# Performance work log

Measured on AMD Instinct MI355X. Metric: run time of the kernel, lower is better.

The kernel has to match this reference:

```python
import jax, jax.numpy as jnp
from jax import lax
import numpy as np

N, I, O = 64, 8, 8
B = 512
S_EX, S_PHI, S_RHO = 10, 60, 60  # S_phi must equal S_rho (alpha loops feed S_rho-sized h into the GRUs)
N_ACTIONS, N_ROLES = 5, 7


def _gru(x, h, Wih, Whh, bih, bhh):
    # torch.nn.GRUCell math
    gi = x @ Wih.T + bih
    gh = h @ Whh.T + bhh
    ir, iz, inn = jnp.split(gi, 3, axis=-1)
    hr, hz, hn = jnp.split(gh, 3, axis=-1)
    r = jax.nn.sigmoid(ir + hr)
    zg = jax.nn.sigmoid(iz + hz)
    n = jnp.tanh(inn + r * hn)
    return (1.0 - zg) * n + zg * h


def setup_inputs() -> dict:
    key = jax.random.key(0)
    ks = jax.random.split(key, 24)
    f32 = jnp.float32
    z = jax.random.normal(ks[0], (B, N, S_EX), f32)
    dz = jax.random.normal(ks[1], (B, N, S_EX), f32)
    has = (jax.random.uniform(ks[2], (B, N)) < 0.9).astype(f32)
    adj = (jnp.triu(jax.random.uniform(ks[3], (N, N)), 1) > 0.7).astype(jnp.int32)

    def lin(k, o, i):
        return (jax.random.normal(k, (o, i), f32) * np.float32(1.0 / np.sqrt(i)))

    d = dict(z=z, dz=dz, has=has, adj=adj)
    d['Wih_f'] = lin(ks[4], 3 * S_PHI, S_RHO)
    d['Whh_f'] = lin(ks[5], 3 * S_PHI, S_PHI)
    d['bih_f'] = jax.random.normal(ks[6], (3 * S_PHI,), f32) * 0.02
    d['bhh_f'] = jax.random.normal(ks[7], (3 * S_PHI,), f32) * 0.02
    d['Wih_b'] = lin(ks[8], 3 * S_PHI, S_RHO)
    d['Whh_b'] = lin(ks[9], 3 * S_PHI, S_PHI)
    d['bih_b'] = jax.random.normal(ks[10], (3 * S_PHI,), f32) * 0.02
    d['bhh_b'] = jax.random.normal(ks[11], (3 * S_PHI,), f32) * 0.02
    d['Wf'] = lin(ks[12], S_RHO, S_PHI + 2 * S_EX)
    d['bf'] = jax.random.normal(ks[13], (S_RHO,), f32) * 0.02
    d['Wb'] = lin(ks[14], S_RHO, S_PHI + 2 * S_EX)
    d['bb'] = jax.random.normal(ks[15], (S_RHO,), f32) * 0.02
    d['Wa'] = lin(ks[16], N_ACTIONS, 2 * S_PHI)
    d['ba'] = jax.random.normal(ks[17], (N_ACTIONS,), f32) * 0.02
    d['Wc'] = lin(ks[18], 1, 2 * S_PHI)
    d['bc'] = jax.random.normal(ks[19], (1,), f32) * 0.02
    d['Wu'] = lin(ks[20], N_ROLES, 2 * S_RHO)
    d['bu'] = jax.random.normal(ks[21], (N_ROLES,), f32) * 0.02
    return d


def reference(z, dz, has, adj,
              Wih_f, Whh_f, bih_f, bhh_f,
              Wih_b, Whh_b, bih_b, bhh_b,
              Wf, bf, Wb, bb, Wa, ba, Wc, bc, Wu, bu):
    Bn, Nn = has.shape
    dt = z.dtype
    adjf = adj.astype(dt)

    # ---- forward sweep over nodes in ascending order ----
    def fwd_outer(rho, i):
        def inner(h, j):
            hn = _gru(rho[j], h, Wih_f, Whh_f, bih_f, bhh_f)
            blend = adjf[j, i] * has[:, j][:, None]  # edge exists AND source node present
            return h + blend * (hn - h), None
        h, _ = lax.scan(inner, jnp.zeros((Bn, S_PHI), dt), jnp.arange(Nn))
        rho_i = jnp.tanh(jnp.concatenate([h, z[:, i], dz[:, i]], 1) @ Wf.T + bf)
        return rho.at[i].set(rho_i), None

    rho_f, _ = lax.scan(fwd_outer, jnp.zeros((Nn, Bn, S_RHO), dt), jnp.arange(Nn))

    # ---- backward sweep over nodes in descending order ----
    def bwd_outer(rho, i):
        def inner(h, j):
            hn = _gru(rho[j], h, Wih_b, Whh_b, bih_b, bhh_b)
            blend = adjf[i, j] * has[:, j][:, None]  # out-edges of i, visited descending
            return h + blend * (hn - h), None
        h, _ = lax.scan(inner, jnp.zeros((Bn, S_PHI), dt), jnp.arange(Nn - 1, -1, -1))
        rho_i = jnp.concatenate([h, z[:, i], dz[:, i]], 1) @ Wb.T + bb
        return rho.at[i].set(rho_i), None

    rho_b, _ = lax.scan(bwd_outer, jnp.zeros((Nn, Bn, S_RHO), dt), jnp.arange(Nn - 1, -1, -1))

    # ---- aggregate outputs (last O nodes) and inputs (first I nodes) ----
    h = jnp.zeros((Bn, S_RHO), dt)
    for i in range(N - O, N):
        hn = _gru(rho_f[i], h, Wih_f, Whh_f, bih_f, bhh_f)
        h = h + has[:, i][:, None] * (hn - h)
    alpha_f = h
    h = jnp.zeros((Bn, S_RHO), dt)
    for i in reversed(range(I)):
        hn = _gru(rho_b[i], h, Wih_b, Whh_b, bih_b, bhh_b)
        h = h + has[:, i][:, None] * (hn - h)
    alpha_b = h

    ab = jnp.concatenate([alpha_f, alpha_b], 1)
    omega = ab @ Wa.T + ba          # [B, 5]
    value = ab @ Wc.T + bc          # [B, 1]

    feats = jnp.concatenate([rho_f, rho_b], -1)           # [N, B, 2*S_rho]
    psi = jnp.einsum('nbs,rs->brn', feats, Wu) + bu[None, :, None]  # [B, 7, N]
    m = has[:, None, :]
    psi = -60.0 * (1.0 - m) + psi * m  # interpolate(-60, psi, has)

    instr_prob = jax.nn.softmax(omega, axis=1)
    role_prob = jax.nn.softmax(psi, axis=2)
    return instr_prob, role_prob, value
```

## Files before the change

### kernel.cpp

```cpp
#include <hip/hip_runtime.h>
#include <hip/hip_bf16.h>

#define NN 64
#define BATCH 512
#define SP 60
#define SG 180
#define SEX 10
#define CATD 80
#define NA 5
#define NR 7
#define OO 8
#define II 8

typedef unsigned long long u64;
typedef unsigned short u16;
typedef unsigned int u32;
typedef unsigned char u8;

#define OFF_Z     0
#define OFF_DZ    327680
#define OFF_HAS   655360
#define OFF_WIHF  688128
#define OFF_WHHF  698928
#define OFF_BIHF  709728
#define OFF_BHHF  709908
#define OFF_WIHB  710088
#define OFF_WHHB  720888
#define OFF_BIHB  731688
#define OFF_BHHB  731868
#define OFF_WF    732048
#define OFF_BF    736848
#define OFF_WB    736908
#define OFF_BB    741708
#define OFF_WA    741768
#define OFF_BA    742368
#define OFF_WC    742373
#define OFF_BC    742493
#define OFF_WU    742494
#define OFF_BU    743334
#define CONV_TOTAL 743341
#define OFF_FLAG  743342
#define OFF_RHOF  743344
#define OFF_RHOB  (OFF_RHOF + 1966080)
#define OFF_ALF   (OFF_RHOB + 1966080)
#define OFF_ALB   (OFF_ALF + 30720)
#define OUT_TOTAL 232448

typedef _Float16 f16;
typedef _Float16 half2_t __attribute__((ext_vector_type(2)));
typedef _Float16 f16x8 __attribute__((ext_vector_type(8)));
typedef float f32x4 __attribute__((ext_vector_type(4)));

__device__ __forceinline__ float us2f(u16 v){
  return __uint_as_float(((u32)v) << 16);
}
__device__ __forceinline__ u16 f2bf(float f){
  __hip_bfloat16 h = __float2bfloat16(f);
  return *reinterpret_cast<u16*>(&h);
}
__device__ __forceinline__ float rcp_(float x){ return __builtin_amdgcn_rcpf(x); }
__device__ __forceinline__ float sigm(float x){
  return rcp_(1.f + __expf(-x));
}
__device__ __forceinline__ float tanh_(float x){
  float e = __expf(2.f*fabsf(x));
  float t = 1.f - 2.f*rcp_(e + 1.f);
  return copysignf(t, x);
}
__device__ __forceinline__ u32 pack2(float a, float b){
  half2_t h; h[0] = (f16)a; h[1] = (f16)b;
  return __builtin_bit_cast(u32, h);
}
__device__ __forceinline__ float fdot2_(u32 a, u32 b, float c){
  return __builtin_amdgcn_fdot2(__builtin_bit_cast(half2_t, a),
                                __builtin_bit_cast(half2_t, b), c, false);
}
__device__ __forceinline__ f16x8 bc16(uint4 v){ return __builtin_bit_cast(f16x8, v); }
__device__ __forceinline__ f32x4 mfma16(f16x8 a, f16x8 b, f32x4 c){
  return __builtin_amdgcn_mfma_f32_16x16x32_f16(a, b, c, 0, 0, 0);
}

struct HP { uint4 q[8]; };
__device__ __forceinline__ u32 hpc(const HP& p, int k){
  const uint4& v = p.q[k>>2];
  switch(k&3){ case 0: return v.x; case 1: return v.y; case 2: return v.z; default: return v.w; }
}

__device__ __forceinline__ int detect_bf16(const u32* w){
  int f = 0;
  for (int i=0;i<256;i++) f |= (w[i] == 0x3F803F80u) ? 1 : 0;
  return f;
}

__global__ __launch_bounds__(256) void conv_in(
  const void* z, const void* dz, const void* has,
  const void* WihF, const void* WhhF, const void* bihF, const void* bhhF,
  const void* WihB, const void* WhhB, const void* bihB, const void* bhhB,
  const void* Wf_, const void* bf_, const void* Wb_, const void* bb_,
  const void* Wa, const void* ba, const void* Wc, const void* bc,
  const void* Wu, const void* bu, float* ws)
{
  const int isbf = detect_bf16((const u32*)has);
  if (blockIdx.x == 0 && threadIdx.x == 0) ws[OFF_FLAG] = (float)isbf;
  int idx = blockIdx.x*256 + threadIdx.x;
  if (idx >= CONV_TOTAL) return;
  const void* src; int loc;
  if      (idx < OFF_DZ  ){ src=z;    loc=idx-OFF_Z;    }
  else if (idx < OFF_HAS ){ src=dz;   loc=idx-OFF_DZ;   }
  else if (idx < OFF_WIHF){ src=has;  loc=idx-OFF_HAS;  }
  else if (idx < OFF_WHHF){ src=WihF; loc=idx-OFF_WIHF; }
  else if (idx < OFF_BIHF){ src=WhhF; loc=idx-OFF_WHHF; }
  else if (idx < OFF_BHHF){ src=bihF; loc=idx-OFF_BIHF; }
  else if (idx < OFF_WIHB){ src=bhhF; loc=idx-OFF_BHHF; }
  else if (idx < OFF_WHHB){ src=WihB; loc=idx-OFF_WIHB; }
  else if (idx < OFF_BIHB){ src=WhhB; loc=idx-OFF_WHHB; }
  else if (idx < OFF_BHHB){ src=bihB; loc=idx-OFF_BIHB; }
  else if (idx < OFF_WF  ){ src=bhhB; loc=idx-OFF_BHHB; }
  else if (idx < OFF_BF  ){ src=Wf_;  loc=idx-OFF_WF;   }
  else if (idx < OFF_WB  ){ src=bf_;  loc=idx-OFF_BF;   }
  else if (idx < OFF_BB  ){ src=Wb_;  loc=idx-OFF_WB;   }
  else if (idx < OFF_WA  ){ src=bb_;  loc=idx-OFF_BB;   }
  else if (idx < OFF_BA  ){ src=Wa;   loc=idx-OFF_WA;   }
  else if (idx < OFF_WC  ){ src=ba;   loc=idx-OFF_BA;   }
  else if (idx < OFF_BC  ){ src=Wc;   loc=idx-OFF_WC;   }
  else if (idx < OFF_WU  ){ src=bc;   loc=idx-OFF_BC;   }
  else if (idx < OFF_BU  ){ src=Wu;   loc=idx-OFF_WU;   }
  else                    { src=bu;   loc=idx-OFF_BU;   }
  float v = isbf ? us2f(((const u16*)src)[loc]) : ((const float*)src)[loc];
  ws[idx] = v;
}

__global__ __launch_bounds__(128, 2) void dir_kernel(const int* __restrict__ adj,
                                                     float* __restrict__ ws)
{
  const int tid = threadIdx.x;
  const int w   = tid >> 6;
  const int u   = tid & 63;
  const int ml  = u & 15;
  const int q   = u >> 4;
  const int bid = blockIdx.x;
  const int bwd = bid >> 9;
  const int b   = bid & 511;

  const float* Wih  = ws + (bwd ? OFF_WIHB : OFF_WIHF);
  const float* Whh  = ws + (bwd ? OFF_WHHB : OFF_WHHF);
  const float* bih  = ws + (bwd ? OFF_BIHB : OFF_BIHF);
  const float* bhh  = ws + (bwd ? OFF_BHHB : OFF_BHHF);
  const float* Wcat = ws + (bwd ? OFF_WB   : OFF_WF);
  const float* bcat = ws + (bwd ? OFF_BB   : OFF_BF);
  const float* zc   = ws + OFF_Z;
  const float* dzc  = ws + OFF_DZ;
  const float* hasc = ws + OFF_HAS;
  float* rho   = ws + (bwd ? OFF_RHOB : OFF_RHOF);
  float* alpha = ws + (bwd ? OFF_ALB  : OFF_ALF);

  __shared__ uint4 sH4[65][9];
  __shared__ uint4 sRhoPad[8];
  __shared__ uint4 sRhoHist[8][8];
  __shared__ float sRhoOut[NN][SP];
  __shared__ u32 sZp[NN][5];
  __shared__ u32 sDZp[NN][5];
  __shared__ float sHas[NN];
  __shared__ u64 sRowM[NN];
  __shared__ u8 sConsL[NN][64];
  __shared__ int sConsCnt[NN];

  #define ROWB(I) ((char*)&sH4[(I)][0])
  const u32 BIASW = 0x3C000000u;

  {
    if (tid < 64){
      u64 rowm = 0;
      for (int j=0;j<64;j++) rowm |= ((u64)(adj[tid*64+j]!=0))<<j;
      sRowM[tid] = rowm;
      sHas[tid] = hasc[b*NN + tid];
    }
    for (int idx=tid; idx<65*9; idx+=128){
      uint4 v = {0,0,0,0};
      if (idx % 9 == 7) v.w = BIASW;
      ((uint4*)sH4)[idx] = v;
    }
    if (tid < 8){ uint4 v={0,0,0,0}; if (tid==7) v.w = BIASW; sRhoPad[tid]=v; }
    if (tid < 64){ uint4 v={0,0,0,0}; if ((tid&7)==7) v.w = BIASW; ((uint4*)sRhoHist)[tid]=v; }
    for (int idx=tid; idx<NN*5; idx+=128){
      int n2=idx/5, p2=idx%5;
      sZp [n2][p2] = pack2(zc [(size_t)b*NN*SEX + n2*SEX + 2*p2],
                           zc [(size_t)b*NN*SEX + n2*SEX + 2*p2+1]);
      sDZp[n2][p2] = pack2(dzc[(size_t)b*NN*SEX + n2*SEX + 2*p2],
                           dzc[(size_t)b*NN*SEX + n2*SEX + 2*p2+1]);
    }
  }
  __syncthreads();
  if (tid < 64){
    u64 cm = 0;
    if (bwd) for (int i2=0;i2<64;i2++) cm |= ((sRowM[i2]>>tid)&1ULL)<<i2;
    u64 m = bwd ? cm : sRowM[tid];
    int c = 0;
    while (m){ int i2 = (int)__builtin_ctzll(m); m &= m-1; sConsL[tid][c++] = (u8)i2; }
    sConsCnt[tid] = c;
  }

  f16x8 Ar[2][4], Az[2][4], Anh[2][2], Ani[2][2];
  #pragma unroll
  for (int mtl=0; mtl<2; mtl++){
    const int mt = 2*w + mtl;
    const int R = 16*mt + ml;
    const bool rok = (R < SP);
    #pragma unroll
    for (int kt=0; kt<4; kt++){
      f16x8 vr, vz;
      #pragma unroll
      for (int j=0;j<8;j++){
        const int K = 32*kt + 8*q + j;
        float wr=0.f, wz=0.f;
        if (rok){
          if (K < SP){ wr = Whh[R*SP+K]; wz = Whh[(60+R)*SP+K]; }
          else if (K >= 64 && K < 64+SP){ wr = Wih[R*SP+(K-64)]; wz = Wih[(60+R)*SP+(K-64)]; }
          else if (K == 127){ wr = bhh[R]+bih[R]; wz = bhh[60+R]+bih[60+R]; }
        }
        vr[j]=(f16)wr; vz[j]=(f16)wz;
      }
      Ar[mtl][kt]=vr; Az[mtl][kt]=vz;
    }
    #pragma unroll
    for (int kt=0; kt<2; kt++){
      f16x8 vn, vi;
      #pragma unroll
      for (int j=0;j<8;j++){
        const int K = 32*kt + 8*q + j;
        float wn=0.f, wi=0.f;
        if (rok){
          if (K < SP){ wn = Whh[(120+R)*SP+K]; wi = Wih[(120+R)*SP+K]; }
          else if (K == 63){ wn = bhh[120+R]; wi = bih[120+R]; }
        }
        vn[j]=(f16)wn; vi[j]=(f16)wi;
      }
      Anh[mtl][kt]=vn; Ani[mtl][kt]=vi;
    }
  }

  u32 wc[40];
  float bct = 0.f;
  if (w == 0){
    #pragma unroll
    for (int k=0;k<40;k++) wc[k] = pack2(Wcat[u*CATD + 2*k], Wcat[u*CATD + 2*k+1]);
    bct = bcat[u];
  }
  __syncthreads();

  auto gatepass = [&](f16x8 Bh0, f16x8 Bh1, f16x8 Br0, f16x8 Br1,
                      const f32x4* Gn, int ci, bool wr, float bl){
    f32x4 Dr[2], Dz[2], Dn[2];
    #pragma unroll
    for (int mtl=0;mtl<2;mtl++){
      f32x4 a={0,0,0,0};
      a = mfma16(Ar[mtl][0], Bh0, a); a = mfma16(Ar[mtl][1], Bh1, a);
      a = mfma16(Ar[mtl][2], Br0, a); a = mfma16(Ar[mtl][3], Br1, a);
      Dr[mtl] = a;
      f32x4 c2={0,0,0,0};
      c2 = mfma16(Az[mtl][0], Bh0, c2); c2 = mfma16(Az[mtl][1], Bh1, c2);
      c2 = mfma16(Az[mtl][2], Br0, c2); c2 = mfma16(Az[mtl][3], Br1, c2);
      Dz[mtl] = c2;
      f32x4 d={0,0,0,0};
      d = mfma16(Anh[mtl][0], Bh0, d); d = mfma16(Anh[mtl][1], Bh1, d);
      Dn[mtl] = d;
    }
    #pragma unroll
    for (int mtl=0;mtl<2;mtl++){
      const int mt = 2*w + mtl;
      char* rp = ROWB(ci) + 32*mt + 8*q;
      uint2 h2 = *(uint2*)rp;
      half2_t ha = __builtin_bit_cast(half2_t, h2.x);
      half2_t hb = __builtin_bit_cast(half2_t, h2.y);
      float hold[4] = { (float)ha[0], (float)ha[1], (float)hb[0], (float)hb[1] };
      float hw[4];
      #pragma unroll
      for (int reg=0;reg<4;reg++){
        float r_ = sigm(Dr[mtl][reg]);
        float zg = sigm(Dz[mtl][reg]);
        float nv = tanh_(Gn[mtl][reg] + r_*Dn[mtl][reg]);
        float hn_ = (1.f - zg)*nv + zg*hold[reg];
        hw[reg] = (bl != 0.f) ? hn_ : hold[reg];
      }
      if (wr && !(mt==3 && q==3)){
        uint2 o; o.x = pack2(hw[0],hw[1]); o.y = pack2(hw[2],hw[3]);
        *(uint2*)rp = o;
      }
    }
  };

  int t = bwd ? 63 : 0;
  const int dt = bwd ? -1 : 1;
  for (int s=0; s<64; s++, t+=dt){
    if (w == 0){
      HP ht;
      { const uint4* _r=(const uint4*)&sH4[t][0];
        #pragma unroll
        for (int _k=0;_k<8;_k++) ht.q[_k]=_r[_k]; }
      float c0 = bct, c1 = 0.f, c2 = 0.f, c3 = 0.f;
      #pragma unroll
      for (int k=0;k<28;k+=4){
        c0 = fdot2_(wc[k],   hpc(ht,k),   c0);
        c1 = fdot2_(wc[k+1], hpc(ht,k+1), c1);
        c2 = fdot2_(wc[k+2], hpc(ht,k+2), c2);
        c3 = fdot2_(wc[k+3], hpc(ht,k+3), c3);
      }
      c0 = fdot2_(wc[28], hpc(ht,28), c0);
      c1 = fdot2_(wc[29], hpc(ht,29), c1);
      #pragma unroll
      for (int p2=0;p2<5;p2++){
        c2 = fdot2_(wc[30+p2], sZp [t][p2], c2);
        c3 = fdot2_(wc[35+p2], sDZp[t][p2], c3);
      }
      float acc = (c0 + c1) + (c2 + c3);
      float rv = bwd ? acc : tanh_(acc);
      if (u < SP){
        sRhoOut[t][u] = rv;
        *(f16*)((char*)&sRhoPad[0] + 2*u) = (f16)rv;
      }
      const int slot = bwd ? t : (t - (NN-OO));
      if (slot >= 0 && slot < 8 && u < SP)
        *(f16*)((char*)&sRhoHist[slot][0] + 2*u) = (f16)rv;
    }
    __syncthreads();

    const float blendT = sHas[t];
    const int cnt = sConsCnt[t];
    if (blendT != 0.f && cnt > 0){
      const f16x8 Br0 = bc16(sRhoPad[q]);
      const f16x8 Br1 = bc16(sRhoPad[4+q]);
      f32x4 Gn[2];
      #pragma unroll
      for (int mtl=0;mtl<2;mtl++){
        f32x4 g={0,0,0,0};
        g = mfma16(Ani[mtl][0], Br0, g);
        g = mfma16(Ani[mtl][1], Br1, g);
        Gn[mtl] = g;
      }
      const int np = (cnt + 15) >> 4;
      for (int p=0; p<np; p++){
        const int idxp = 16*p + ml;
        const int ci = (idxp < cnt) ? (int)sConsL[t][idxp] : 64;
        const f16x8 Bh0 = bc16(sH4[ci][q]);
        const f16x8 Bh1 = bc16(sH4[ci][4+q]);
        __syncthreads();
        gatepass(Bh0, Bh1, Br0, Br1, Gn, ci, idxp < cnt, 1.0f);
      }
    }
    __syncthreads();
  }

  for (int idx=tid; idx<NN*SP; idx+=128){
    int n2 = idx/SP, s2 = idx%SP;
    rho[((size_t)n2*BATCH + b)*SP + s2] = sRhoOut[n2][s2];
  }

  for (int s2=0; s2<8; s2++){
    const int i = bwd ? (7 - s2) : (NN - OO + s2);
    const int slot = bwd ? i : (i - (NN-OO));
    const f16x8 Th0 = bc16(sH4[64][q]);
    const f16x8 Th1 = bc16(sH4[64][4+q]);
    const f16x8 Tr0 = bc16(sRhoHist[slot][q]);
    const f16x8 Tr1 = bc16(sRhoHist[slot][4+q]);
    f32x4 Gt[2];
    #pragma unroll
    for (int mtl=0;mtl<2;mtl++){
      f32x4 g={0,0,0,0};
      g = mfma16(Ani[mtl][0], Tr0, g);
      g = mfma16(Ani[mtl][1], Tr1, g);
      Gt[mtl] = g;
    }
    __syncthreads();
    gatepass(Th0, Th1, Tr0, Tr1, Gt, 64, ml==0, sHas[i]);
    __syncthreads();
  }
  if (tid < SP) alpha[(size_t)b*SP + tid] = (float)*(const f16*)(ROWB(64) + 2*tid);
  #undef ROWB
}

__global__ __launch_bounds__(256, 1) void head_kernel(float* __restrict__ ws,
                                                      void* __restrict__ outp)
{
  const int b = blockIdx.x;
  const int tid = threadIdx.x;
  const int isbf = (ws[OFF_FLAG] != 0.f);
  const float* hasc   = ws + OFF_HAS;
  const float* WaC    = ws + OFF_WA;
  const float* baC    = ws + OFF_BA;
  const float* WcC    = ws + OFF_WC;
  const float* bcC    = ws + OFF_BC;
  const float* WuC    = ws + OFF_WU;
  const float* buC    = ws + OFF_BU;
  const float* rhoF   = ws + OFF_RHOF;
  const float* rhoB   = ws + OFF_RHOB;
  const float* alphaF = ws + OFF_ALF;
  const float* alphaB = ws + OFF_ALB;

  __shared__ float sF[NN][121];
  __shared__ float sAB[120];
  __shared__ float sWu[NR*120];
  __shared__ float sHasR[NN];
  __shared__ float sPsi[NR][NN];
  __shared__ float sRed[NR][2];
  __shared__ float sOm[NA];

  auto wout = [&](int idx, float v){
    if (isbf) ((u16*)outp)[idx] = f2bf(v);
    else      ((float*)outp)[idx] = v;
  };

  for (int idx=tid; idx<NN*SP; idx+=256){
    int n = idx/SP, s = idx%SP;
    sF[n][s]    = rhoF[((size_t)n*BATCH + b)*SP + s];
    sF[n][60+s] = rhoB[((size_t)n*BATCH + b)*SP + s];
  }
  for (int idx=tid; idx<120; idx+=256)
    sAB[idx] = (idx<60) ? alphaF[(size_t)b*SP + idx] : alphaB[(size_t)b*SP + idx-60];
  for (int idx=tid; idx<NR*120; idx+=256) sWu[idx] = WuC[idx];
  for (int idx=tid; idx<NN; idx+=256) sHasR[idx] = hasc[b*NN + idx];
  __syncthreads();

  for (int idx=tid; idx<NR*NN; idx+=256){
    int r = idx/NN, n = idx%NN;
    float acc = buC[r];
    for (int s=0;s<120;s++) acc += sF[n][s]*sWu[r*120+s];
    sPsi[r][n] = (sHasR[n] != 0.f) ? acc : -60.f;
  }
  if (tid >= 64 && tid < 64+NA){
    int a = tid - 64;
    float acc = baC[a];
    for (int s=0;s<120;s++) acc += sAB[s]*WaC[a*120+s];
    sOm[a] = acc;
  }
  if (tid == 70){
    float acc = bcC[0];
    for (int s=0;s<120;s++) acc += sAB[s]*WcC[s];
    wout(2560 + BATCH*NR*NN + b, acc);
  }
  __syncthreads();

  if (tid < NR){
    float m = -1e30f;
    for (int n=0;n<NN;n++) m = fmaxf(m, sPsi[tid][n]);
    float ssum = 0.f;
    for (int n=0;n<NN;n++) ssum += __expf(sPsi[tid][n]-m);
    sRed[tid][0] = m; sRed[tid][1] = 1.f/ssum;
  }
  if (tid == 8){
    float m = -1e30f;
    for (int a=0;a<NA;a++) m = fmaxf(m, sOm[a]);
    float e[NA]; float ssum = 0.f;
    for (int a=0;a<NA;a++){ e[a] = __expf(sOm[a]-m); ssum += e[a]; }
    for (int a=0;a<NA;a++) wout(b*NA + a, e[a]/ssum);
  }
  __syncthreads();

  for (int idx=tid; idx<NR*NN; idx+=256){
    int r = idx/NN, n = idx%NN;
    float v = __expf(sPsi[r][n]-sRed[r][0]) * sRed[r][1];
    wout(2560 + (size_t)b*NR*NN + idx, v);
  }
}

extern "C" void kernel_launch(void* const* d_in, const int* in_sizes, int n_in,
                              void* d_out, int out_size, void* d_ws, size_t ws_size,
                              hipStream_t stream)
{
  const int* adj = (const int*)d_in[3];
  float* ws = (float*)d_ws;

  conv_in<<<(CONV_TOTAL+255)/256, 256, 0, stream>>>(
      d_in[0], d_in[1], d_in[2],
      d_in[4], d_in[5], d_in[6], d_in[7],
      d_in[8], d_in[9], d_in[10], d_in[11],
      d_in[12], d_in[13], d_in[14], d_in[15],
      d_in[16], d_in[17], d_in[18], d_in[19],
      d_in[20], d_in[21], ws);

  dir_kernel<<<1024, 128, 0, stream>>>(adj, ws);

  head_kernel<<<512, 256, 0, stream>>>(ws, d_out);
}
```

Measured before the change: 274.3 us.

## Split GRU gate row tiles across four waves instead of two per block

Doubles the dir_kernel block from 128 to 256 threads, so each of four waves owns one 16-row MFMA tile instead of two. This halves the per-wave MFMA and gate-activation work on the serial recurrence critical path and the weight registers each wave holds. In exchange, every __syncthreads now has twice as many waves to coordinate, and the launch bounds of 256 threads with 4 blocks per unit may force register limits.

Result: slower. 281.9 us (+2.8%).

```diff
diff --git a/kernel.cpp b/kernel.cpp
--- a/kernel.cpp
+++ b/kernel.cpp
@@ -130,7 +130,7 @@
   ws[idx] = v;
 }
 
-__global__ __launch_bounds__(128, 2) void dir_kernel(const int* __restrict__ adj,
+__global__ __launch_bounds__(256, 4) void dir_kernel(const int* __restrict__ adj,
                                                      float* __restrict__ ws)
 {
   const int tid = threadIdx.x;
@@ -175,14 +175,14 @@
       sRowM[tid] = rowm;
       sHas[tid] = hasc[b*NN + tid];
     }
-    for (int idx=tid; idx<65*9; idx+=128){
+    for (int idx=tid; idx<65*9; idx+=256){
       uint4 v = {0,0,0,0};
       if (idx % 9 == 7) v.w = BIASW;
       ((uint4*)sH4)[idx] = v;
     }
     if (tid < 8){ uint4 v={0,0,0,0}; if (tid==7) v.w = BIASW; sRhoPad[tid]=v; }
     if (tid < 64){ uint4 v={0,0,0,0}; if ((tid&7)==7) v.w = BIASW; ((uint4*)sRhoHist)[tid]=v; }
-    for (int idx=tid; idx<NN*5; idx+=128){
+    for (int idx=tid; idx<NN*5; idx+=256){
       int n2=idx/5, p2=idx%5;
       sZp [n2][p2] = pack2(zc [(size_t)b*NN*SEX + n2*SEX + 2*p2],
                            zc [(size_t)b*NN*SEX + n2*SEX + 2*p2+1]);
@@ -200,11 +200,9 @@
     sConsCnt[tid] = c;
   }
 
-  f16x8 Ar[2][4], Az[2][4], Anh[2][2], Ani[2][2];
-  #pragma unroll
-  for (int mtl=0; mtl<2; mtl++){
-    const int mt = 2*w + mtl;
-    const int R = 16*mt + ml;
+  f16x8 Ar[4], Az[4], Anh[2], Ani[2];
+  {
+    const int R = 16*w + ml;
     const bool rok = (R < SP);
     #pragma unroll
     for (int kt=0; kt<4; kt++){
@@ -220,7 +218,7 @@
         }
         vr[j]=(f16)wr; vz[j]=(f16)wz;
       }
-      Ar[mtl][kt]=vr; Az[mtl][kt]=vz;
+      Ar[kt]=vr; Az[kt]=vz;
     }
     #pragma unroll
     for (int kt=0; kt<2; kt++){
@@ -235,7 +233,7 @@
         }
         vn[j]=(f16)wn; vi[j]=(f16)wi;
       }
-      Anh[mtl][kt]=vn; Ani[mtl][kt]=vi;
+      Anh[kt]=vn; Ani[kt]=vi;
     }
   }
 
@@ -249,43 +247,31 @@
   __syncthreads();
 
   auto gatepass = [&](f16x8 Bh0, f16x8 Bh1, f16x8 Br0, f16x8 Br1,
-                      const f32x4* Gn, int ci, bool wr, float bl){
-    f32x4 Dr[2], Dz[2], Dn[2];
+                      f32x4 Gn, int ci, bool wr, float bl){
+    f32x4 Dr={0,0,0,0}, Dz={0,0,0,0}, Dn={0,0,0,0};
+    Dr = mfma16(Ar[0], Bh0, Dr); Dr = mfma16(Ar[1], Bh1, Dr);
+    Dr = mfma16(Ar[2], Br0, Dr); Dr = mfma16(Ar[3], Br1, Dr);
+    Dz = mfma16(Az[0], Bh0, Dz); Dz = mfma16(Az[1], Bh1, Dz);
+    Dz = mfma16(Az[2], Br0, Dz); Dz = mfma16(Az[3], Br1, Dz);
+    Dn = mfma16(Anh[0], Bh0, Dn); Dn = mfma16(Anh[1], Bh1, Dn);
+
+    char* rp = ROWB(ci) + 32*w + 8*q;
+    uint2 h2 = *(uint2*)rp;
+    half2_t ha = __builtin_bit_cast(half2_t, h2.x);
+    half2_t hb = __builtin_bit_cast(half2_t, h2.y);
+    float hold[4] = { (float)ha[0], (float)ha[1], (float)hb[0], (float)hb[1] };
+    float hw[4];
     #pragma unroll
-    for (int mtl=0;mtl<2;mtl++){
-      f32x4 a={0,0,0,0};
-      a = mfma16(Ar[mtl][0], Bh0, a); a = mfma16(Ar[mtl][1], Bh1, a);
-      a = mfma16(Ar[mtl][2], Br0, a); a = mfma16(Ar[mtl][3], Br1, a);
-      Dr[mtl] = a;
-      f32x4 c2={0,0,0,0};
-      c2 = mfma16(Az[mtl][0], Bh0, c2); c2 = mfma16(Az[mtl][1], Bh1, c2);
-      c2 = mfma16(Az[mtl][2], Br0, c2); c2 = mfma16(Az[mtl][3], Br1, c2);
-      Dz[mtl] = c2;
-      f32x4 d={0,0,0,0};
-      d = mfma16(Anh[mtl][0], Bh0, d); d = mfma16(Anh[mtl][1], Bh1, d);
-      Dn[mtl] = d;
-    }
-    #pragma unroll
-    for (int mtl=0;mtl<2;mtl++){
-      const int mt = 2*w + mtl;
-      char* rp = ROWB(ci) + 32*mt + 8*q;
-      uint2 h2 = *(uint2*)rp;
-      half2_t ha = __builtin_bit_cast(half2_t, h2.x);
-      half2_t hb = __builtin_bit_cast(half2_t, h2.y);
-      float hold[4] = { (float)ha[0], (float)ha[1], (float)hb[0], (float)hb[1] };
-      float hw[4];
-      #pragma unroll
-      for (int reg=0;reg<4;reg++){
-        float r_ = sigm(Dr[mtl][reg]);
-        float zg = sigm(Dz[mtl][reg]);
-        float nv = tanh_(Gn[mtl][reg] + r_*Dn[mtl][reg]);
-        float hn_ = (1.f - zg)*nv + zg*hold[reg];
-        hw[reg] = (bl != 0.f) ? hn_ : hold[reg];
-      }
-      if (wr && !(mt==3 && q==3)){
-        uint2 o; o.x = pack2(hw[0],hw[1]); o.y = pack2(hw[2],hw[3]);
-        *(uint2*)rp = o;
-      }
+    for (int reg=0;reg<4;reg++){
+      float r_ = sigm(Dr[reg]);
+      float zg = sigm(Dz[reg]);
+      float nv = tanh_(Gn[reg] + r_*Dn[reg]);
+      float hn_ = (1.f - zg)*nv + zg*hold[reg];
+      hw[reg] = (bl != 0.f) ? hn_ : hold[reg];
+    }
+    if (wr && !(w==3 && q==3)){
+      uint2 o; o.x = pack2(hw[0],hw[1]); o.y = pack2(hw[2],hw[3]);
+      *(uint2*)rp = o;
     }
   };
 
@@ -329,14 +315,9 @@
     if (blendT != 0.f && cnt > 0){
       const f16x8 Br0 = bc16(sRhoPad[q]);
       const f16x8 Br1 = bc16(sRhoPad[4+q]);
-      f32x4 Gn[2];
-      #pragma unroll
-      for (int mtl=0;mtl<2;mtl++){
-        f32x4 g={0,0,0,0};
-        g = mfma16(Ani[mtl][0], Br0, g);
-        g = mfma16(Ani[mtl][1], Br1, g);
-        Gn[mtl] = g;
-      }
+      f32x4 Gn={0,0,0,0};
+      Gn = mfma16(Ani[0], Br0, Gn);
+      Gn = mfma16(Ani[1], Br1, Gn);
       const int np = (cnt + 15) >> 4;
       for (int p=0; p<np; p++){
         const int idxp = 16*p + ml;
@@ -350,7 +331,7 @@
     __syncthreads();
   }
 
-  for (int idx=tid; idx<NN*SP; idx+=128){
+  for (int idx=tid; idx<NN*SP; idx+=256){
     int n2 = idx/SP, s2 = idx%SP;
     rho[((size_t)n2*BATCH + b)*SP + s2] = sRhoOut[n2][s2];
   }
@@ -362,14 +343,9 @@
     const f16x8 Th1 = bc16(sH4[64][4+q]);
     const f16x8 Tr0 = bc16(sRhoHist[slot][q]);
     const f16x8 Tr1 = bc16(sRhoHist[slot][4+q]);
-    f32x4 Gt[2];
-    #pragma unroll
-    for (int mtl=0;mtl<2;mtl++){
-      f32x4 g={0,0,0,0};
-      g = mfma16(Ani[mtl][0], Tr0, g);
-      g = mfma16(Ani[mtl][1], Tr1, g);
-      Gt[mtl] = g;
-    }
+    f32x4 Gt={0,0,0,0};
+    Gt = mfma16(Ani[0], Tr0, Gt);
+    Gt = mfma16(Ani[1], Tr1, Gt);
     __syncthreads();
     gatepass(Th0, Th1, Tr0, Tr1, Gt, 64, ml==0, sHas[i]);
     __syncthreads();
@@ -477,7 +453,7 @@
       d_in[16], d_in[17], d_in[18], d_in[19],
       d_in[20], d_in[21], ws);
 
-  dir_kernel<<<1024, 128, 0, stream>>>(adj, ws);
+  dir_kernel<<<1024, 256, 0, stream>>>(adj, ws);
 
   head_kernel<<<512, 256, 0, stream>>>(ws, d_out);
 }
```
